# Kernel optimization log

Hardware: AMD Instinct MI355X
Metric: run time of the kernel (lower is better)

Reference implementation:

```python
import jax, jax.numpy as jnp
import numpy as np

VOCAB = 100000
EMB = 256
HID = 512
H = HID // 2            # per-direction hidden size
T_LEN = 2048
N_TAGS = 7
START, END = 5, 6
NEG = -10000.0


def setup_inputs() -> dict:
    key = jax.random.key(0)
    ks = jax.random.split(key, 16)
    n = lambda k, sh: jax.random.normal(k, sh, dtype=jnp.float32)
    bound = 1.0 / np.sqrt(H)  # torch LSTM/Linear-style init scale
    u = lambda k, sh: jax.random.uniform(k, sh, dtype=jnp.float32, minval=-bound, maxval=bound)
    transitions = n(ks[12], (N_TAGS, N_TAGS))
    transitions = transitions.at[:, START].set(NEG).at[END, :].set(NEG)
    return {
        "words": jax.random.randint(ks[0], (T_LEN,), 0, VOCAB),
        "embed": n(ks[1], (VOCAB + 1, EMB)),
        "W_ih_f": u(ks[2], (4 * H, EMB)),
        "W_hh_f": u(ks[3], (4 * H, H)),
        "b_ih_f": u(ks[4], (4 * H,)),
        "b_hh_f": u(ks[5], (4 * H,)),
        "W_ih_b": u(ks[6], (4 * H, EMB)),
        "W_hh_b": u(ks[7], (4 * H, H)),
        "b_ih_b": u(ks[8], (4 * H,)),
        "b_hh_b": u(ks[9], (4 * H,)),
        "W_out": u(ks[10], (N_TAGS, HID)),
        "b_out": u(ks[11], (N_TAGS,)),
        "transitions": transitions,
        "h0": n(ks[13], (2, H)),
        "c0": n(ks[14], (2, H)),
    }


def _lstm_dir(xs, h0, c0, Wih, Whh, bih, bhh):
    # xs: [T, EMB]; torch gate order i, f, g, o
    def step(carry, x):
        h, c = carry
        g = x @ Wih.T + bih + h @ Whh.T + bhh  # [4H]
        i, f, gg, o = jnp.split(g, 4)
        i, f, o = jax.nn.sigmoid(i), jax.nn.sigmoid(f), jax.nn.sigmoid(o)
        c = f * c + i * jnp.tanh(gg)
        h = o * jnp.tanh(c)
        return (h, c), h
    _, hs = jax.lax.scan(step, (h0, c0), xs)
    return hs  # [T, H]


def _features(words, embed, W_ih_f, W_hh_f, b_ih_f, b_hh_f,
              W_ih_b, W_hh_b, b_ih_b, b_hh_b, W_out, b_out, h0, c0):
    xs = embed[words]                                   # [T, EMB]
    hs_f = _lstm_dir(xs, h0[0], c0[0], W_ih_f, W_hh_f, b_ih_f, b_hh_f)
    hs_b = _lstm_dir(xs[::-1], h0[1], c0[1], W_ih_b, W_hh_b, b_ih_b, b_hh_b)[::-1]
    lstm_out = jnp.concatenate([hs_f, hs_b], axis=1)    # [T, HID]
    return lstm_out @ W_out.T + b_out                   # [T, N_TAGS]


def _viterbi(feats, transitions):
    init = jnp.full((N_TAGS,), NEG, dtype=feats.dtype).at[START].set(0.0)

    def vit_step(fv, feat):
        # torch code: next_tag_var[j] = forward_var + transitions[j]
        M = fv[None, :] + transitions          # [j, i] = fv[i] + T[j, i]
        bp = jnp.argmax(M, axis=1)             # [N_TAGS] best prev tag
        fv_new = jnp.max(M, axis=1) + feat
        return fv_new, bp

    fv, bptrs = jax.lax.scan(vit_step, init, feats)     # bptrs: [T, N_TAGS]
    terminal = fv + transitions[END]
    final_tag = jnp.argmax(terminal)
    path_score = terminal[final_tag]

    def back_step(tag, bp):
        return bp[tag], tag
    _start, path = jax.lax.scan(back_step, final_tag, bptrs, reverse=True)
    return path_score, path  # path: [T] tag ids (B/I/E/S/N = 0..4)


def reference(words, embed, W_ih_f, W_hh_f, b_ih_f, b_hh_f,
              W_ih_b, W_hh_b, b_ih_b, b_hh_b, W_out, b_out,
              transitions, h0, c0):
    feats = _features(words, embed, W_ih_f, W_hh_f, b_ih_f, b_hh_f,
                      W_ih_b, W_hh_b, b_ih_b, b_hh_b, W_out, b_out, h0, c0)
    return _viterbi(feats, transitions)
```

## Files before the change

### kernel.cpp

```cpp
#include <hip/hip_runtime.h>

typedef unsigned int u32;

#define T_LEN 2048
#define NEG (-10000.0f)
#define WSCALE 2032.0f
#define HSCALE 127.0f
#define SCALE_INV (1.0f / (2032.0f * 127.0f))

__device__ __forceinline__ int sdot4(u32 a, u32 b, int c) {
#if __has_builtin(__builtin_amdgcn_sdot4)
  return __builtin_amdgcn_sdot4((int)a, (int)b, c, false);
#else
  int r = c;
  r += (int)(signed char)(a)       * (int)(signed char)(b);
  r += (int)(signed char)(a >> 8)  * (int)(signed char)(b >> 8);
  r += (int)(signed char)(a >> 16) * (int)(signed char)(b >> 16);
  r += (int)(signed char)(a >> 24) * (int)(signed char)(b >> 24);
  return r;
#endif
}

__device__ __forceinline__ u32 rdlane_u32(u32 v, int lane) {
#if __has_builtin(__builtin_amdgcn_readlane)
  return (u32)__builtin_amdgcn_readlane((int)v, lane);
#else
  return (u32)__shfl((int)v, lane);
#endif
}

__device__ __forceinline__ float rdlane_f32(float v, int lane) {
  return __builtin_bit_cast(float, rdlane_u32(__builtin_bit_cast(u32, v), lane));
}

__device__ __forceinline__ void block_sync_lds() {
  asm volatile("s_waitcnt lgkmcnt(0)" ::: "memory");
  __builtin_amdgcn_s_barrier();
}

#define PIN8(a,b,c_,d_,e,f,g_,h_)                                     \
  asm volatile("" : "+v"(a), "+v"(b), "+v"(c_), "+v"(d_),             \
                    "+v"(e), "+v"(f), "+v"(g_), "+v"(h_))
#define PINROW(W, base) \
  PIN8(W[base+0], W[base+1], W[base+2], W[base+3],                    \
       W[base+4], W[base+5], W[base+6], W[base+7])

__global__ void pack_whh_i8(const float* __restrict__ Wf,
                            const float* __restrict__ Wb,
                            u32* __restrict__ WP) {
  int idx = blockIdx.x * 256 + threadIdx.x;
  int d   = idx >> 16;
  int G   = (idx >> 14) & 3;
  int q4  = (idx >> 10) & 15;
  int c   = (idx >> 2) & 255;
  int j   = idx & 3;
  const float* W = d ? Wb : Wf;
  float4 v = *(const float4*)&W[(G * 256 + c) * 256 + q4 * 16 + j * 4];
  int b0 = (int)rintf(fminf(fmaxf(v.x * WSCALE, -127.f), 127.f));
  int b1 = (int)rintf(fminf(fmaxf(v.y * WSCALE, -127.f), 127.f));
  int b2 = (int)rintf(fminf(fmaxf(v.z * WSCALE, -127.f), 127.f));
  int b3 = (int)rintf(fminf(fmaxf(v.w * WSCALE, -127.f), 127.f));
  WP[(((d * 4 + G) * 16 + q4) * 256 + c) * 4 + j] =
      (u32)(b0 & 255) | ((u32)(b1 & 255) << 8) |
      ((u32)(b2 & 255) << 16) | ((u32)(b3 & 255) << 24);
}

__global__ void gather_kernel(const int* __restrict__ words,
                              const float* __restrict__ embed,
                              float* __restrict__ xs) {
  int t = blockIdx.x;
  int k = threadIdx.x;
  xs[t * 256 + k] = embed[(size_t)words[t] * 256 + k];
}

__global__ __launch_bounds__(256) void gemm_xw(
    const float* __restrict__ xs,
    const float* __restrict__ Wf, const float* __restrict__ Wb,
    const float* __restrict__ bihf, const float* __restrict__ bhhf,
    const float* __restrict__ bihb, const float* __restrict__ bhhb,
    float* __restrict__ XW) {
  __shared__ float lx[32 * 256];
  __shared__ float lw[32 * 132];
  const int tid = threadIdx.x;
  const int t0 = blockIdx.x * 32;
  const int g0 = blockIdx.y * 128;
  const int d  = blockIdx.z;
  const float* W = d ? Wb : Wf;

  #pragma unroll 4
  for (int r = 0; r < 32; ++r) lx[r * 256 + tid] = xs[(t0 + r) * 256 + tid];

  const int tg = tid & 31, tt = tid >> 5;
  float acc[4][4] = {};

  for (int kc = 0; kc < 8; ++kc) {
    __syncthreads();
    #pragma unroll
    for (int r2 = 0; r2 < 16; ++r2) {
      int gg = r2 * 8 + (tid >> 5);
      int k  = tid & 31;
      lw[k * 132 + gg] = W[(g0 + gg) * 256 + kc * 32 + k];
    }
    __syncthreads();
    #pragma unroll
    for (int k = 0; k < 32; ++k) {
      float4 wv = *(const float4*)&lw[k * 132 + tg * 4];
      #pragma unroll
      for (int a = 0; a < 4; ++a) {
        float xa = lx[(tt * 4 + a) * 256 + kc * 32 + k];
        acc[a][0] = fmaf(xa, wv.x, acc[a][0]);
        acc[a][1] = fmaf(xa, wv.y, acc[a][1]);
        acc[a][2] = fmaf(xa, wv.z, acc[a][2]);
        acc[a][3] = fmaf(xa, wv.w, acc[a][3]);
      }
    }
  }
  const float* bih = d ? bihb : bihf;
  const float* bhh = d ? bhhb : bhhf;
  int gcol = g0 + tg * 4;
  float bb[4];
  #pragma unroll
  for (int j = 0; j < 4; ++j) bb[j] = bih[gcol + j] + bhh[gcol + j];
  #pragma unroll
  for (int a = 0; a < 4; ++a) {
    size_t trow = (size_t)d * T_LEN + t0 + tt * 4 + a;
    #pragma unroll
    for (int j = 0; j < 4; ++j) {
      int g = gcol + j;
      XW[trow * 1024 + (g & 255) * 4 + (g >> 8)] = acc[a][j] + bb[j];
    }
  }
}

__global__ void __launch_bounds__(256)
__attribute__((amdgpu_waves_per_eu(1, 1)))
lstm_seq(
    const float* __restrict__ XW, float* __restrict__ HS,
    const u32* __restrict__ wpack,
    const float* __restrict__ h0, const float* __restrict__ c0) {
  __shared__ u32 H8[2][64];
  const int tid = threadIdx.x;
  const int d = blockIdx.x;
  const int lane = tid & 63;

  u32 wI[64], wF[64], wG[64], wO[64];
  {
    const uint4* wr = (const uint4*)wpack;
    #pragma unroll
    for (int q4 = 0; q4 < 16; ++q4) {
      uint4 t;
      t = wr[((d * 4 + 0) * 16 + q4) * 256 + tid];
      wI[q4*4+0] = t.x; wI[q4*4+1] = t.y; wI[q4*4+2] = t.z; wI[q4*4+3] = t.w;
      t = wr[((d * 4 + 1) * 16 + q4) * 256 + tid];
      wF[q4*4+0] = t.x; wF[q4*4+1] = t.y; wF[q4*4+2] = t.z; wF[q4*4+3] = t.w;
      t = wr[((d * 4 + 2) * 16 + q4) * 256 + tid];
      wG[q4*4+0] = t.x; wG[q4*4+1] = t.y; wG[q4*4+2] = t.z; wG[q4*4+3] = t.w;
      t = wr[((d * 4 + 3) * 16 + q4) * 256 + tid];
      wO[q4*4+0] = t.x; wO[q4*4+1] = t.y; wO[q4*4+2] = t.z; wO[q4*4+3] = t.w;
    }
  }

  float c = c0[d * 256 + tid];
  float h = h0[d * 256 + tid];
  {
    int hi = (int)rintf(fminf(fmaxf(h, -1.0f), 1.0f) * HSCALE);
    ((unsigned char*)&H8[0][0])[tid] = (unsigned char)(hi & 255);
  }
  block_sync_lds();
  u32 hA = H8[0][lane];

  const int delta = d ? -1024 : 1024;
  const float* xwp = XW + ((size_t)d * T_LEN + (d ? (T_LEN - 1) : 0)) * 1024 + tid * 4;
  float4 xc = *(const float4*)xwp;

  for (int s = 0; s < T_LEN; ++s) {
    float4 xn = make_float4(0.f, 0.f, 0.f, 0.f);
    if (s < T_LEN - 1) { xwp += delta; xn = *(const float4*)xwp; }

    PINROW(wI, 0);  PINROW(wI, 8);  PINROW(wI, 16); PINROW(wI, 24);
    PINROW(wI, 32); PINROW(wI, 40); PINROW(wI, 48); PINROW(wI, 56);
    PINROW(wF, 0);  PINROW(wF, 8);  PINROW(wF, 16); PINROW(wF, 24);
    PINROW(wF, 32); PINROW(wF, 40); PINROW(wF, 48); PINROW(wF, 56);
    PINROW(wG, 0);  PINROW(wG, 8);  PINROW(wG, 16); PINROW(wG, 24);
    PINROW(wG, 32); PINROW(wG, 40); PINROW(wG, 48); PINROW(wG, 56);

    int aI = 0, aF = 0, aG = 0, aO = 0;
    #pragma unroll
    for (int q = 0; q < 16; ++q) {
      u32 s0 = rdlane_u32(hA, 4*q+0), s1 = rdlane_u32(hA, 4*q+1),
          s2 = rdlane_u32(hA, 4*q+2), s3 = rdlane_u32(hA, 4*q+3);
      aI = sdot4(wI[4*q+0], s0, aI); aF = sdot4(wF[4*q+0], s0, aF);
      aG = sdot4(wG[4*q+0], s0, aG); aO = sdot4(wO[4*q+0], s0, aO);
      aI = sdot4(wI[4*q+1], s1, aI); aF = sdot4(wF[4*q+1], s1, aF);
      aG = sdot4(wG[4*q+1], s1, aG); aO = sdot4(wO[4*q+1], s1, aO);
      aI = sdot4(wI[4*q+2], s2, aI); aF = sdot4(wF[4*q+2], s2, aF);
      aG = sdot4(wG[4*q+2], s2, aG); aO = sdot4(wO[4*q+2], s2, aO);
      aI = sdot4(wI[4*q+3], s3, aI); aF = sdot4(wF[4*q+3], s3, aF);
      aG = sdot4(wG[4*q+3], s3, aG); aO = sdot4(wO[4*q+3], s3, aO);
    }

    float gi = fmaf((float)aI, SCALE_INV, xc.x);
    float gf = fmaf((float)aF, SCALE_INV, xc.y);
    float gc = fmaf((float)aG, SCALE_INV, xc.z);
    float go = fmaf((float)aO, SCALE_INV, xc.w);
    gi = 1.0f / (1.0f + __expf(-gi));
    gf = 1.0f / (1.0f + __expf(-gf));
    go = 1.0f / (1.0f + __expf(-go));
    gc = 1.0f - 2.0f / (__expf(2.0f * gc) + 1.0f);
    c = gf * c + gi * gc;
    float th = 1.0f - 2.0f / (__expf(2.0f * c) + 1.0f);
    h = go * th;

    const int t = d ? (T_LEN - 1 - s) : s;
    HS[((size_t)d * T_LEN + t) * 256 + tid] = h;

    int hi = (int)rintf(h * HSCALE);
    const int wbuf = (s + 1) & 1;
    ((unsigned char*)&H8[wbuf][0])[tid] = (unsigned char)(hi & 255);
    block_sync_lds();
    hA = H8[wbuf][lane];
    xc = xn;
  }
}

__global__ void feats_kernel(const float* __restrict__ hs,
                             const float* __restrict__ wout,
                             const float* __restrict__ bout,
                             float* __restrict__ feats) {
  __shared__ float lf[16 * 257];
  __shared__ float lb[16 * 257];
  const int tid = threadIdx.x;
  const int t0 = blockIdx.x * 16;
  for (int i = tid; i < 16 * 256; i += 128) {
    int r = i >> 8, k = i & 255;
    lf[r * 257 + k] = hs[(size_t)(t0 + r) * 256 + k];
    lb[r * 257 + k] = hs[(size_t)T_LEN * 256 + (size_t)(t0 + r) * 256 + k];
  }
  __syncthreads();
  const int tl = tid >> 3, n = tid & 7;
  if (n < 7) {
    float acc = bout[n];
    #pragma unroll 8
    for (int k = 0; k < 256; ++k) acc = fmaf(lf[tl * 257 + k], wout[n * 512 + k], acc);
    #pragma unroll 8
    for (int k = 0; k < 256; ++k) acc = fmaf(lb[tl * 257 + k], wout[n * 512 + 256 + k], acc);
    feats[(t0 + tl) * 7 + n] = acc;
  }
}

__global__ __launch_bounds__(256) void viterbi_kernel(
    const float* __restrict__ feats,
    const float* __restrict__ trans,
    float* __restrict__ out) {
  extern __shared__ char vsm[];
  float*         fe = (float*)vsm;
  unsigned char* bp = (unsigned char*)(vsm + 57344);
  unsigned char* G  = (unsigned char*)(vsm + 73728);
  unsigned char* bt = (unsigned char*)(vsm + 73984);
  const int tid = threadIdx.x;

  for (int i = tid; i < T_LEN * 7; i += 256) fe[i] = feats[i];
  __syncthreads();

  if (tid < 64) {
    const int j  = tid;
    const int jc = (j < 7) ? j : 0;
    float Trow[7];
    #pragma unroll
    for (int i = 0; i < 7; ++i) Trow[i] = trans[jc * 7 + i];
    float fv = (j == 5) ? 0.0f : NEG;
    for (int t = 0; t < T_LEN; ++t) {
      float f0 = rdlane_f32(fv, 0), f1 = rdlane_f32(fv, 1), f2 = rdlane_f32(fv, 2),
            f3 = rdlane_f32(fv, 3), f4 = rdlane_f32(fv, 4), f5 = rdlane_f32(fv, 5),
            f6 = rdlane_f32(fv, 6);
      float v0 = f0 + Trow[0], v1 = f1 + Trow[1], v2 = f2 + Trow[2],
            v3 = f3 + Trow[3], v4 = f4 + Trow[4], v5 = f5 + Trow[5],
            v6 = f6 + Trow[6];
      bool c01 = v0 >= v1;  float m01 = c01 ? v0 : v1;  int i01 = c01 ? 0 : 1;
      bool c23 = v2 >= v3;  float m23 = c23 ? v2 : v3;  int i23 = c23 ? 2 : 3;
      bool c45 = v4 >= v5;  float m45 = c45 ? v4 : v5;  int i45 = c45 ? 4 : 5;
      bool cA  = m01 >= m23; float mA = cA ? m01 : m23; int iA = cA ? i01 : i23;
      bool cB  = m45 >= v6;  float mB = cB ? m45 : v6;  int iB = cB ? i45 : 6;
      bool cF  = mA >= mB;   float best = cF ? mA : mB; int bi = cF ? iA : iB;
      if (j < 7) bp[t * 8 + j] = (unsigned char)bi;
      fv = best + fe[t * 7 + jc];
    }
    float term = fv + trans[42 + jc];
    float best = rdlane_f32(term, 0); int btag = 0;
    #pragma unroll
    for (int i = 1; i < 7; ++i) {
      float ti = rdlane_f32(term, i);
      if (ti > best) { best = ti; btag = i; }
    }
    if (j == 0) {
      out[0] = best;
      bt[31] = (unsigned char)btag;
    }
  }
  __syncthreads();

  {
    const int s = tid >> 3, j = tid & 7;
    if (s < 32 && j < 7) {
      int g = j;
      for (int t = s * 64 + 63; t >= s * 64; --t) g = bp[t * 8 + g];
      G[s * 8 + j] = (unsigned char)g;
    }
  }
  __syncthreads();

  if (tid == 0) {
    int x = bt[31];
    for (int s = 31; s >= 1; --s) { x = G[s * 8 + x]; bt[s - 1] = (unsigned char)x; }
  }
  __syncthreads();

  if (tid < 32) {
    const int s = tid;
    int tag = bt[s];
    for (int t = s * 64 + 63; t >= s * 64; --t) {
      out[1 + t] = (float)tag;
      tag = bp[t * 8 + tag];
    }
  }
}

extern "C" void kernel_launch(void* const* d_in, const int* in_sizes, int n_in,
                              void* d_out, int out_size, void* d_ws, size_t ws_size,
                              hipStream_t stream) {
  const int*   words = (const int*)d_in[0];
  const float* embed = (const float*)d_in[1];
  const float* Wih_f = (const float*)d_in[2];
  const float* Whh_f = (const float*)d_in[3];
  const float* bih_f = (const float*)d_in[4];
  const float* bhh_f = (const float*)d_in[5];
  const float* Wih_b = (const float*)d_in[6];
  const float* Whh_b = (const float*)d_in[7];
  const float* bih_b = (const float*)d_in[8];
  const float* bhh_b = (const float*)d_in[9];
  const float* Wout  = (const float*)d_in[10];
  const float* bout  = (const float*)d_in[11];
  const float* trans = (const float*)d_in[12];
  const float* h0    = (const float*)d_in[13];
  const float* c0    = (const float*)d_in[14];

  float* ws = (float*)d_ws;
  float* XW = ws;
  float* HS = ws + 4194304;
  float* XS = ws + 5242880;
  float* FE = ws + 5767168;
  u32*   WP = (u32*)(ws + 5781504);

  pack_whh_i8<<<512, 256, 0, stream>>>(Whh_f, Whh_b, WP);
  gather_kernel<<<T_LEN, 256, 0, stream>>>(words, embed, XS);
  dim3 ggrid(T_LEN / 32, 1024 / 128, 2);
  gemm_xw<<<ggrid, 256, 0, stream>>>(XS, Wih_f, Wih_b, bih_f, bhh_f, bih_b, bhh_b, XW);
  lstm_seq<<<2, 256, 0, stream>>>(XW, HS, WP, h0, c0);
  feats_kernel<<<128, 128, 0, stream>>>(HS, Wout, bout, FE);
  viterbi_kernel<<<1, 256, 74048, stream>>>(FE, trans, (float*)d_out);
}
```

Baseline: 2.627 ms.

## Split LSTM recurrence over 512 threads with hybrid register/LDS weight storage

The sequential LSTM kernel now runs 512 threads per direction instead of 256. Each thread computes two of the four gates for one hidden unit: the lower half does input/forget and the upper half does cell/output. Each thread keeps 144 of its 256 input columns of int8 weights in registers and streams the remaining 112 from LDS every step. This halves the serial sdot4 chain per thread and reduces register pressure, at the cost of an extra barrier and an LDS exchange of gate sums each timestep, plus per-step LDS weight reads.

```diff
diff --git a/kernel.cpp b/kernel.cpp
--- a/kernel.cpp
+++ b/kernel.cpp
@@ -7,6 +7,13 @@
 #define WSCALE 2032.0f
 #define HSCALE 127.0f
 #define SCALE_INV (1.0f / (2032.0f * 127.0f))
+
+#define RQ 9
+#define WSTRIDE 60
+#define WR_DWORDS 73728
+#define SM_GT 30720
+#define SM_H8 31232
+#define SM_TOT 31296
 
 __device__ __forceinline__ int sdot4(u32 a, u32 b, int c) {
 #if __has_builtin(__builtin_amdgcn_sdot4)
@@ -38,31 +45,43 @@
   __builtin_amdgcn_s_barrier();
 }
 
-#define PIN8(a,b,c_,d_,e,f,g_,h_)                                     \
-  asm volatile("" : "+v"(a), "+v"(b), "+v"(c_), "+v"(d_),             \
-                    "+v"(e), "+v"(f), "+v"(g_), "+v"(h_))
-#define PINROW(W, base) \
-  PIN8(W[base+0], W[base+1], W[base+2], W[base+3],                    \
-       W[base+4], W[base+5], W[base+6], W[base+7])
-
 __global__ void pack_whh_i8(const float* __restrict__ Wf,
                             const float* __restrict__ Wb,
                             u32* __restrict__ WP) {
   int idx = blockIdx.x * 256 + threadIdx.x;
-  int d   = idx >> 16;
-  int G   = (idx >> 14) & 3;
-  int q4  = (idx >> 10) & 15;
-  int c   = (idx >> 2) & 255;
-  int j   = idx & 3;
+  int d, r, kbase;
+  if (idx < WR_DWORDS) {
+    int e = idx & 3;
+    int t = (idx >> 2) & 511;
+    int v = idx >> 11;
+    d = v / 18;
+    int u = v - d * 18;
+    int half = t >> 8, cc = t & 255;
+    int sub = (u < 9) ? 0 : 1;
+    int q4  = sub ? (u - 9) : u;
+    r = (2 * half + sub) * 256 + cc;
+    kbase = q4 * 16 + e * 4;
+  } else {
+    int rem = idx - WR_DWORDS;
+    int w = rem / 56;
+    int j = rem - w * 56;
+    d = w >> 9;
+    int t = w & 511;
+    int half = t >> 8, cc = t & 255;
+    int sub = (j < 28) ? 0 : 1;
+    int jj  = sub ? (j - 28) : j;
+    r = (2 * half + sub) * 256 + cc;
+    kbase = 144 + jj * 4;
+  }
   const float* W = d ? Wb : Wf;
-  float4 v = *(const float4*)&W[(G * 256 + c) * 256 + q4 * 16 + j * 4];
-  int b0 = (int)rintf(fminf(fmaxf(v.x * WSCALE, -127.f), 127.f));
-  int b1 = (int)rintf(fminf(fmaxf(v.y * WSCALE, -127.f), 127.f));
-  int b2 = (int)rintf(fminf(fmaxf(v.z * WSCALE, -127.f), 127.f));
-  int b3 = (int)rintf(fminf(fmaxf(v.w * WSCALE, -127.f), 127.f));
-  WP[(((d * 4 + G) * 16 + q4) * 256 + c) * 4 + j] =
-      (u32)(b0 & 255) | ((u32)(b1 & 255) << 8) |
-      ((u32)(b2 & 255) << 16) | ((u32)(b3 & 255) << 24);
+  u32 p = 0;
+  #pragma unroll
+  for (int b = 0; b < 4; ++b) {
+    float v = W[r * 256 + kbase + b];
+    int q = (int)rintf(fminf(fmaxf(v * WSCALE, -127.f), 127.f));
+    p |= (u32)(q & 255) << (8 * b);
+  }
+  WP[idx] = p;
 }
 
 __global__ void gather_kernel(const int* __restrict__ words,
@@ -132,93 +151,102 @@
   }
 }
 
-__global__ void __launch_bounds__(256)
-__attribute__((amdgpu_waves_per_eu(1, 1)))
+__global__ void __launch_bounds__(512, 2)
+__attribute__((amdgpu_waves_per_eu(2, 2)))
 lstm_seq(
     const float* __restrict__ XW, float* __restrict__ HS,
     const u32* __restrict__ wpack,
     const float* __restrict__ h0, const float* __restrict__ c0) {
-  __shared__ u32 H8[2][64];
-  const int tid = threadIdx.x;
+  extern __shared__ u32 smem[];
+  const int t = threadIdx.x;
   const int d = blockIdx.x;
-  const int lane = tid & 63;
-
-  u32 wI[64], wF[64], wG[64], wO[64];
+  const int lane = t & 63;
+  const int c = t & 255;
+  const bool lower = (t < 256);
+
+  {
+    const u32* wlg = wpack + WR_DWORDS + (d * 512 + t) * 56;
+    #pragma unroll
+    for (int j = 0; j < 56; ++j) smem[t * WSTRIDE + j] = wlg[j];
+  }
+  uint4 WA[RQ], WB[RQ];
   {
     const uint4* wr = (const uint4*)wpack;
     #pragma unroll
-    for (int q4 = 0; q4 < 16; ++q4) {
-      uint4 t;
-      t = wr[((d * 4 + 0) * 16 + q4) * 256 + tid];
-      wI[q4*4+0] = t.x; wI[q4*4+1] = t.y; wI[q4*4+2] = t.z; wI[q4*4+3] = t.w;
-      t = wr[((d * 4 + 1) * 16 + q4) * 256 + tid];
-      wF[q4*4+0] = t.x; wF[q4*4+1] = t.y; wF[q4*4+2] = t.z; wF[q4*4+3] = t.w;
-      t = wr[((d * 4 + 2) * 16 + q4) * 256 + tid];
-      wG[q4*4+0] = t.x; wG[q4*4+1] = t.y; wG[q4*4+2] = t.z; wG[q4*4+3] = t.w;
-      t = wr[((d * 4 + 3) * 16 + q4) * 256 + tid];
-      wO[q4*4+0] = t.x; wO[q4*4+1] = t.y; wO[q4*4+2] = t.z; wO[q4*4+3] = t.w;
-    }
-  }
-
-  float c = c0[d * 256 + tid];
-  float h = h0[d * 256 + tid];
-  {
-    int hi = (int)rintf(fminf(fmaxf(h, -1.0f), 1.0f) * HSCALE);
-    ((unsigned char*)&H8[0][0])[tid] = (unsigned char)(hi & 255);
+    for (int u = 0; u < RQ; ++u) {
+      WA[u] = wr[(d * 18 + u) * 512 + t];
+      WB[u] = wr[(d * 18 + 9 + u) * 512 + t];
+    }
+  }
+  int2* GT2 = (int2*)(smem + SM_GT);
+  u32*  H8  = smem + SM_H8;
+
+  float cst = 0.f, h = 0.f;
+  if (lower) {
+    cst = c0[d * 256 + c];
+    h   = h0[d * 256 + c];
+    int hi = (int)rintf(fminf(fmaxf(h, -1.f), 1.f) * HSCALE);
+    ((unsigned char*)H8)[c] = (unsigned char)(hi & 255);
   }
   block_sync_lds();
-  u32 hA = H8[0][lane];
+  u32 hA = H8[lane];
 
   const int delta = d ? -1024 : 1024;
-  const float* xwp = XW + ((size_t)d * T_LEN + (d ? (T_LEN - 1) : 0)) * 1024 + tid * 4;
-  float4 xc = *(const float4*)xwp;
+  const float* xwp = XW + ((size_t)d * T_LEN + (d ? (T_LEN - 1) : 0)) * 1024 + c * 4;
+  float4 xc = make_float4(0.f, 0.f, 0.f, 0.f);
+  if (lower) xc = *(const float4*)xwp;
 
   for (int s = 0; s < T_LEN; ++s) {
     float4 xn = make_float4(0.f, 0.f, 0.f, 0.f);
-    if (s < T_LEN - 1) { xwp += delta; xn = *(const float4*)xwp; }
-
-    PINROW(wI, 0);  PINROW(wI, 8);  PINROW(wI, 16); PINROW(wI, 24);
-    PINROW(wI, 32); PINROW(wI, 40); PINROW(wI, 48); PINROW(wI, 56);
-    PINROW(wF, 0);  PINROW(wF, 8);  PINROW(wF, 16); PINROW(wF, 24);
-    PINROW(wF, 32); PINROW(wF, 40); PINROW(wF, 48); PINROW(wF, 56);
-    PINROW(wG, 0);  PINROW(wG, 8);  PINROW(wG, 16); PINROW(wG, 24);
-    PINROW(wG, 32); PINROW(wG, 40); PINROW(wG, 48); PINROW(wG, 56);
-
-    int aI = 0, aF = 0, aG = 0, aO = 0;
-    #pragma unroll
-    for (int q = 0; q < 16; ++q) {
-      u32 s0 = rdlane_u32(hA, 4*q+0), s1 = rdlane_u32(hA, 4*q+1),
-          s2 = rdlane_u32(hA, 4*q+2), s3 = rdlane_u32(hA, 4*q+3);
-      aI = sdot4(wI[4*q+0], s0, aI); aF = sdot4(wF[4*q+0], s0, aF);
-      aG = sdot4(wG[4*q+0], s0, aG); aO = sdot4(wO[4*q+0], s0, aO);
-      aI = sdot4(wI[4*q+1], s1, aI); aF = sdot4(wF[4*q+1], s1, aF);
-      aG = sdot4(wG[4*q+1], s1, aG); aO = sdot4(wO[4*q+1], s1, aO);
-      aI = sdot4(wI[4*q+2], s2, aI); aF = sdot4(wF[4*q+2], s2, aF);
-      aG = sdot4(wG[4*q+2], s2, aG); aO = sdot4(wO[4*q+2], s2, aO);
-      aI = sdot4(wI[4*q+3], s3, aI); aF = sdot4(wF[4*q+3], s3, aF);
-      aG = sdot4(wG[4*q+3], s3, aG); aO = sdot4(wO[4*q+3], s3, aO);
-    }
-
-    float gi = fmaf((float)aI, SCALE_INV, xc.x);
-    float gf = fmaf((float)aF, SCALE_INV, xc.y);
-    float gc = fmaf((float)aG, SCALE_INV, xc.z);
-    float go = fmaf((float)aO, SCALE_INV, xc.w);
-    gi = 1.0f / (1.0f + __expf(-gi));
-    gf = 1.0f / (1.0f + __expf(-gf));
-    go = 1.0f / (1.0f + __expf(-go));
-    gc = 1.0f - 2.0f / (__expf(2.0f * gc) + 1.0f);
-    c = gf * c + gi * gc;
-    float th = 1.0f - 2.0f / (__expf(2.0f * c) + 1.0f);
-    h = go * th;
-
-    const int t = d ? (T_LEN - 1 - s) : s;
-    HS[((size_t)d * T_LEN + t) * 256 + tid] = h;
-
-    int hi = (int)rintf(h * HSCALE);
-    const int wbuf = (s + 1) & 1;
-    ((unsigned char*)&H8[wbuf][0])[tid] = (unsigned char)(hi & 255);
+    if (lower && s < T_LEN - 1) { xwp += delta; xn = *(const float4*)xwp; }
+
+    u32 wl_base = t * WSTRIDE;
+    asm("" : "+v"(wl_base));
+
+    int aA = 0, bA = 0, aB = 0, bB = 0;
+    #pragma unroll
+    for (int u = 0; u < RQ; ++u) {
+      u32 s0 = rdlane_u32(hA, 4*u+0), s1 = rdlane_u32(hA, 4*u+1),
+          s2 = rdlane_u32(hA, 4*u+2), s3 = rdlane_u32(hA, 4*u+3);
+      aA = sdot4(WA[u].x, s0, aA); aB = sdot4(WB[u].x, s0, aB);
+      bA = sdot4(WA[u].y, s1, bA); bB = sdot4(WB[u].y, s1, bB);
+      aA = sdot4(WA[u].z, s2, aA); aB = sdot4(WB[u].z, s2, aB);
+      bA = sdot4(WA[u].w, s3, bA); bB = sdot4(WB[u].w, s3, bB);
+    }
+    #pragma unroll
+    for (int q = 0; q < 7; ++q) {
+      uint4 wA = *(const uint4*)&smem[wl_base + 4*q];
+      uint4 wB = *(const uint4*)&smem[wl_base + 28 + 4*q];
+      u32 s0 = rdlane_u32(hA, 36+4*q), s1 = rdlane_u32(hA, 37+4*q),
+          s2 = rdlane_u32(hA, 38+4*q), s3 = rdlane_u32(hA, 39+4*q);
+      aA = sdot4(wA.x, s0, aA); aB = sdot4(wB.x, s0, aB);
+      bA = sdot4(wA.y, s1, bA); bB = sdot4(wB.y, s1, bB);
+      aA = sdot4(wA.z, s2, aA); aB = sdot4(wB.z, s2, aB);
+      bA = sdot4(wA.w, s3, bA); bB = sdot4(wB.w, s3, bB);
+    }
+    if (!lower) GT2[c] = make_int2(aA + bA, aB + bB);
     block_sync_lds();
-    hA = H8[wbuf][lane];
+
+    if (lower) {
+      int2 go2 = GT2[c];
+      float gi = fmaf((float)(aA + bA), SCALE_INV, xc.x);
+      float gf = fmaf((float)(aB + bB), SCALE_INV, xc.y);
+      float gc = fmaf((float)go2.x,    SCALE_INV, xc.z);
+      float go = fmaf((float)go2.y,    SCALE_INV, xc.w);
+      gi = 1.f / (1.f + __expf(-gi));
+      gf = 1.f / (1.f + __expf(-gf));
+      go = 1.f / (1.f + __expf(-go));
+      gc = 1.f - 2.f / (__expf(2.f * gc) + 1.f);
+      cst = gf * cst + gi * gc;
+      float th = 1.f - 2.f / (__expf(2.f * cst) + 1.f);
+      h = go * th;
+      const int tt = d ? (T_LEN - 1 - s) : s;
+      HS[((size_t)d * T_LEN + tt) * 256 + c] = h;
+      int hi = (int)rintf(h * HSCALE);
+      ((unsigned char*)H8)[c] = (unsigned char)(hi & 255);
+    }
+    block_sync_lds();
+    hA = H8[lane];
     xc = xn;
   }
 }
@@ -355,7 +383,7 @@
   gather_kernel<<<T_LEN, 256, 0, stream>>>(words, embed, XS);
   dim3 ggrid(T_LEN / 32, 1024 / 128, 2);
   gemm_xw<<<ggrid, 256, 0, stream>>>(XS, Wih_f, Wih_b, bih_f, bhh_f, bih_b, bhh_b, XW);
-  lstm_seq<<<2, 256, 0, stream>>>(XW, HS, WP, h0, c0);
+  lstm_seq<<<2, 512, SM_TOT * 4, stream>>>(XW, HS, WP, h0, c0);
   feats_kernel<<<128, 128, 0, stream>>>(HS, Wout, bout, FE);
   viterbi_kernel<<<1, 256, 74048, stream>>>(FE, trans, (float*)d_out);
 }
```

After: 4.686 ms. 78.3% more time.
